# Optimization experiments

Measured on AMD Instinct MI355X. Metric: run time of the kernel, lower is better.

The kernel has to match this reference:

```python
import jax, jax.numpy as jnp
import numpy as np

DIM = 768
HEADS = 12
HEAD_DIM = DIM // HEADS
MLP_DIM = 4 * DIM
EPS = 1e-5


def setup_inputs() -> dict:
    key = jax.random.key(0)
    ks = jax.random.split(key, 8)
    s = lambda fan_in: 1.0 / np.sqrt(fan_in)
    return {
        "x": jax.random.normal(ks[0], (2, 2048, DIM), dtype=jnp.float32),
        "ln1_w": jnp.ones((DIM,), jnp.float32),
        "ln1_b": jnp.zeros((DIM,), jnp.float32),
        # weights stored [in, out]
        "qkv_w": jax.random.normal(ks[1], (DIM, 3 * DIM), jnp.float32) * s(DIM),
        "qkv_b": jnp.zeros((3 * DIM,), jnp.float32),
        "proj_w": jax.random.normal(ks[2], (DIM, DIM), jnp.float32) * s(DIM),
        "proj_b": jnp.zeros((DIM,), jnp.float32),
        "ln2_w": jnp.ones((DIM,), jnp.float32),
        "ln2_b": jnp.zeros((DIM,), jnp.float32),
        "lin1_w": jax.random.normal(ks[3], (DIM, MLP_DIM), jnp.float32) * s(DIM),
        "lin1_b": jnp.zeros((MLP_DIM,), jnp.float32),
        "lin2_w": jax.random.normal(ks[4], (MLP_DIM, DIM), jnp.float32) * s(MLP_DIM),
        "lin2_b": jnp.zeros((DIM,), jnp.float32),
    }


def _layernorm(x, w, b):
    mu = jnp.mean(x, axis=-1, keepdims=True)
    var = jnp.mean(jnp.square(x - mu), axis=-1, keepdims=True)
    return (x - mu) * jax.lax.rsqrt(var + EPS) * w + b


def _attention(x, qkv_w, qkv_b, proj_w, proj_b):
    B, N, C = x.shape
    qkv = (x @ qkv_w + qkv_b).reshape(B, N, 3, HEADS, HEAD_DIM)
    q, k, v = qkv[:, :, 0], qkv[:, :, 1], qkv[:, :, 2]  # [B, N, H, Dh]
    scale = HEAD_DIM ** -0.5
    attn = jnp.einsum("bqhd,bkhd->bhqk", q, k) * scale  # full NxN scores
    attn = jax.nn.softmax(attn, axis=-1)
    out = jnp.einsum("bhqk,bkhd->bqhd", attn, v).reshape(B, N, C)
    return out @ proj_w + proj_b


def reference(x, ln1_w, ln1_b, qkv_w, qkv_b, proj_w, proj_b,
              ln2_w, ln2_b, lin1_w, lin1_b, lin2_w, lin2_b):
    x = x + _attention(_layernorm(x, ln1_w, ln1_b), qkv_w, qkv_b, proj_w, proj_b)
    h = _layernorm(x, ln2_w, ln2_b)
    h = jax.nn.gelu(h @ lin1_w + lin1_b, approximate=False) @ lin2_w + lin2_b
    return x + h
```

## Files before the change

### kernel.cpp

```cpp
#include <hip/hip_runtime.h>
#include <hip/hip_bf16.h>
#include <math.h>

#define DIM 768
#define NTOK 4096
#define SEQ 2048
#define HEADS 12
#define HD 64

using bf16x8 = __attribute__((ext_vector_type(8))) __bf16;
using f32x4  = __attribute__((ext_vector_type(4))) float;
typedef unsigned short u16;

__device__ inline u16 f2bf(float f) {
  union { float f; unsigned u; } v; v.f = f;
  unsigned r = v.u + 0x7fffu + ((v.u >> 16) & 1u);
  return (u16)(r >> 16);
}

__device__ inline void pk2bf(float a, float b, u16* o0, u16* o1) {
  union { __hip_bfloat162 h; u16 u[2]; } cv;
  cv.h = __float22bfloat162_rn(make_float2(a, b));
  *o0 = cv.u[0];
  *o1 = cv.u[1];
}

__device__ inline float gelu_t(float x) {
  float z = x * (1.5957691216f + 0.0713548162f * x * x);
  return x / (1.0f + __expf(-z));
}

__device__ inline void gl_lds16(const u16* g, u16* l) {
  __builtin_amdgcn_global_load_lds(
      (const __attribute__((address_space(1))) unsigned int*)g,
      (__attribute__((address_space(3))) unsigned int*)l, 16, 0, 0);
}

__global__ __launch_bounds__(256) void ln_kernel(const float* __restrict__ x,
                                                 const float* __restrict__ w,
                                                 const float* __restrict__ b,
                                                 u16* __restrict__ y) {
  int row = blockIdx.x;
  int t = threadIdx.x;
  const float* xr = x + (size_t)row * DIM;
  float v0 = xr[t], v1 = xr[t + 256], v2 = xr[t + 512];
  float s = v0 + v1 + v2;
  float q = v0 * v0 + v1 * v1 + v2 * v2;
  for (int o = 32; o > 0; o >>= 1) {
    s += __shfl_down(s, o, 64);
    q += __shfl_down(q, o, 64);
  }
  __shared__ float ws_[4], wq_[4], mb[2];
  int wid = t >> 6;
  if ((t & 63) == 0) { ws_[wid] = s; wq_[wid] = q; }
  __syncthreads();
  if (t == 0) {
    float S = ws_[0] + ws_[1] + ws_[2] + ws_[3];
    float Q = wq_[0] + wq_[1] + wq_[2] + wq_[3];
    float mean = S * (1.0f / DIM);
    float var = Q * (1.0f / DIM) - mean * mean;
    mb[0] = mean;
    mb[1] = rsqrtf(var + 1e-5f);
  }
  __syncthreads();
  float mean = mb[0], rstd = mb[1];
  u16* yr = y + (size_t)row * DIM;
  yr[t]       = f2bf((v0 - mean) * rstd * w[t]       + b[t]);
  yr[t + 256] = f2bf((v1 - mean) * rstd * w[t + 256] + b[t + 256]);
  yr[t + 512] = f2bf((v2 - mean) * rstd * w[t + 512] + b[t + 512]);
}

__global__ __launch_bounds__(256) void redln_kernel(
    const float* __restrict__ P0, const float* __restrict__ P1,
    const float* __restrict__ bias, const float* __restrict__ res,
    float* __restrict__ x2, const float* __restrict__ lnw,
    const float* __restrict__ lnb, u16* __restrict__ y) {
  int row = blockIdx.x;
  int t = threadIdx.x;
  size_t off = (size_t)row * DIM;
  float v[3];
#pragma unroll
  for (int k = 0; k < 3; ++k) {
    int c = t + k * 256;
    v[k] = P0[off + c] + P1[off + c] + bias[c] + res[off + c];
    x2[off + c] = v[k];
  }
  float s = v[0] + v[1] + v[2];
  float q = v[0] * v[0] + v[1] * v[1] + v[2] * v[2];
  for (int o = 32; o > 0; o >>= 1) {
    s += __shfl_down(s, o, 64);
    q += __shfl_down(q, o, 64);
  }
  __shared__ float ws_[4], wq_[4], mb[2];
  int wid = t >> 6;
  if ((t & 63) == 0) { ws_[wid] = s; wq_[wid] = q; }
  __syncthreads();
  if (t == 0) {
    float S = ws_[0] + ws_[1] + ws_[2] + ws_[3];
    float Q = wq_[0] + wq_[1] + wq_[2] + wq_[3];
    float mean = S * (1.0f / DIM);
    float var = Q * (1.0f / DIM) - mean * mean;
    mb[0] = mean;
    mb[1] = rsqrtf(var + 1e-5f);
  }
  __syncthreads();
  float mean = mb[0], rstd = mb[1];
#pragma unroll
  for (int k = 0; k < 3; ++k) {
    int c = t + k * 256;
    y[off + c] = f2bf((v[k] - mean) * rstd * lnw[c] + lnb[c]);
  }
}

__global__ __launch_bounds__(256) void wcvt_all(
    const float* __restrict__ W0, const float* __restrict__ W1,
    const float* __restrict__ W2, const float* __restrict__ W3,
    u16* __restrict__ T0, u16* __restrict__ T1,
    u16* __restrict__ T2, u16* __restrict__ T3) {
  int id = blockIdx.x;
  const float* W; u16* Wt; int K, N, local;
  if (id < 1728)      { W = W0; Wt = T0; K = 768;  N = 2304; local = id; }
  else if (id < 2304) { W = W1; Wt = T1; K = 768;  N = 768;  local = id - 1728; }
  else if (id < 4608) { W = W2; Wt = T2; K = 768;  N = 3072; local = id - 2304; }
  else                { W = W3; Wt = T3; K = 3072; N = 768;  local = id - 4608; }
  int ntiles = N / 32;
  int n0 = (local % ntiles) * 32, k0 = (local / ntiles) * 32;
  __shared__ float tile[32][33];
  int tid = threadIdx.x;
  int c = tid & 31, r8 = tid >> 5;
#pragma unroll
  for (int p = 0; p < 4; ++p) {
    int k = r8 + p * 8;
    tile[k][c] = W[(size_t)(k0 + k) * N + n0 + c];
  }
  __syncthreads();
#pragma unroll
  for (int p = 0; p < 4; ++p) {
    int n = r8 + p * 8;
    Wt[(size_t)(n0 + n) * K + k0 + c] = f2bf(tile[c][n]);
  }
}

__global__ __launch_bounds__(256) void vtr_kernel(const u16* __restrict__ qkvB,
                                                  u16* __restrict__ vT) {
  __shared__ u16 tile[32][33];
  int v0 = blockIdx.x * 32, j0 = blockIdx.y * 32, b = blockIdx.z;
  int tid = threadIdx.x;
  int c = tid & 31, r8 = tid >> 5;
#pragma unroll
  for (int p = 0; p < 4; ++p) {
    int r = r8 + p * 8;
    tile[r][c] = qkvB[((size_t)(b * SEQ + j0 + r)) * 2304 + 1536 + v0 + c];
  }
  __syncthreads();
#pragma unroll
  for (int p = 0; p < 4; ++p) {
    int r = r8 + p * 8;
    vT[((size_t)(b * 768 + v0 + r)) * SEQ + j0 + c] = tile[c][r];
  }
}

__global__ __launch_bounds__(256) void bgemm_kernel(
    const u16* __restrict__ A, const u16* __restrict__ Bt,
    const float* __restrict__ bias, u16* __restrict__ Cb,
    int M, int N, int K, int act) {
  __shared__ __align__(16) u16 Asl[128 * 64];
  __shared__ __align__(16) u16 Bsl[128 * 64];
  int tid = threadIdx.x;
  int lane = tid & 63, wave = tid >> 6;
  int wm = wave >> 1, wn = wave & 1;
  int bm = blockIdx.y * 128, bn = blockIdx.x * 128;
  int l15 = lane & 15, quad = lane >> 4;
  int sm8 = tid >> 3;
  int kgx = (tid & 7) ^ (sm8 & 7);

  f32x4 acc[4][4] = {};
  const u16* Ap = A + (size_t)(bm + sm8) * K + kgx * 8;
  const u16* Bp = Bt + (size_t)(bn + sm8) * K + kgx * 8;
  u16* Al = &Asl[(wave * 8) * 64];
  u16* Bl = &Bsl[(wave * 8) * 64];
  int xr = l15 & 7;

  for (int k0 = 0; k0 < K; k0 += 64) {
#pragma unroll
    for (int p = 0; p < 4; ++p)
      gl_lds16(Ap + (size_t)(p * 32) * K + k0, Al + p * 32 * 64);
#pragma unroll
    for (int p = 0; p < 4; ++p)
      gl_lds16(Bp + (size_t)(p * 32) * K + k0, Bl + p * 32 * 64);
    __syncthreads();
#pragma unroll
    for (int ks = 0; ks < 2; ++ks) {
      int pu = ((ks << 2) + quad) ^ xr;
      bf16x8 af[4], bfr[4];
#pragma unroll
      for (int i = 0; i < 4; ++i) {
        af[i]  = *(const bf16x8*)&Asl[(wm * 64 + i * 16 + l15) * 64 + pu * 8];
        bfr[i] = *(const bf16x8*)&Bsl[(wn * 64 + i * 16 + l15) * 64 + pu * 8];
      }
#pragma unroll
      for (int i = 0; i < 4; ++i)
#pragma unroll
        for (int j = 0; j < 4; ++j)
          acc[i][j] = __builtin_amdgcn_mfma_f32_16x16x32_bf16(af[i], bfr[j], acc[i][j], 0, 0, 0);
    }
    __syncthreads();
  }

#pragma unroll
  for (int i = 0; i < 4; ++i) {
#pragma unroll
    for (int j = 0; j < 4; ++j) {
      int n = bn + wn * 64 + j * 16 + l15;
      float bv = bias[n];
      float val[4];
#pragma unroll
      for (int r = 0; r < 4; ++r) {
        float v = acc[i][j][r] + bv;
        val[r] = act ? gelu_t(v) : v;
      }
      u16 c0, c1, c2, c3;
      pk2bf(val[0], val[1], &c0, &c1);
      pk2bf(val[2], val[3], &c2, &c3);
      size_t mbase = (size_t)(bm + wm * 64 + i * 16 + quad * 4) * N + n;
      Cb[mbase]         = c0;
      Cb[mbase + N]     = c1;
      Cb[mbase + 2 * N] = c2;
      Cb[mbase + 3 * N] = c3;
    }
  }
}

__global__ __launch_bounds__(256) void bgemm_splitk(
    const u16* __restrict__ A, const u16* __restrict__ Bt,
    float* __restrict__ P0, float* __restrict__ P1,
    int M, int N, int K) {
  __shared__ __align__(16) u16 Asl[128 * 64];
  __shared__ __align__(16) u16 Bsl[64 * 64];
  int tid = threadIdx.x;
  int lane = tid & 63, wave = tid >> 6;
  int wm = wave >> 1, wn = wave & 1;
  int bm = blockIdx.y * 128, bn = blockIdx.x * 64;
  int l15 = lane & 15, quad = lane >> 4;
  int sm8 = tid >> 3;
  int kgx = (tid & 7) ^ (sm8 & 7);
  int half = K >> 1;
  int kbeg = blockIdx.z * half;

  f32x4 acc[4][2] = {};
  const u16* Ap = A + (size_t)(bm + sm8) * K + kbeg + kgx * 8;
  const u16* Bp = Bt + (size_t)(bn + sm8) * K + kbeg + kgx * 8;
  u16* Al = &Asl[(wave * 8) * 64];
  u16* Bl = &Bsl[(wave * 8) * 64];
  int xr = l15 & 7;

  for (int k0 = 0; k0 < half; k0 += 64) {
#pragma unroll
    for (int p = 0; p < 4; ++p)
      gl_lds16(Ap + (size_t)(p * 32) * K + k0, Al + p * 32 * 64);
#pragma unroll
    for (int p = 0; p < 2; ++p)
      gl_lds16(Bp + (size_t)(p * 32) * K + k0, Bl + p * 32 * 64);
    __syncthreads();
#pragma unroll
    for (int ks = 0; ks < 2; ++ks) {
      int pu = ((ks << 2) + quad) ^ xr;
      bf16x8 af[4], bfr[2];
#pragma unroll
      for (int i = 0; i < 4; ++i)
        af[i] = *(const bf16x8*)&Asl[(wm * 64 + i * 16 + l15) * 64 + pu * 8];
#pragma unroll
      for (int j = 0; j < 2; ++j)
        bfr[j] = *(const bf16x8*)&Bsl[(wn * 32 + j * 16 + l15) * 64 + pu * 8];
#pragma unroll
      for (int i = 0; i < 4; ++i)
#pragma unroll
        for (int j = 0; j < 2; ++j)
          acc[i][j] = __builtin_amdgcn_mfma_f32_16x16x32_bf16(af[i], bfr[j], acc[i][j], 0, 0, 0);
    }
    __syncthreads();
  }

  float* P = blockIdx.z ? P1 : P0;
#pragma unroll
  for (int i = 0; i < 4; ++i) {
#pragma unroll
    for (int j = 0; j < 2; ++j) {
      int n = bn + wn * 32 + j * 16 + l15;
#pragma unroll
      for (int r = 0; r < 4; ++r) {
        int m = bm + wm * 64 + i * 16 + quad * 4 + r;
        P[(size_t)m * N + n] = acc[i][j][r];
      }
    }
  }
}

__global__ __launch_bounds__(256) void red_kernel(
    const float* P0, const float* __restrict__ P1,
    const float* __restrict__ bias, const float* __restrict__ res,
    float* O, int Ncols) {
  int i = blockIdx.x * 256 + threadIdx.x;
  float4 a = ((const float4*)P0)[i];
  float4 b = ((const float4*)P1)[i];
  float4 r = ((const float4*)res)[i];
  int col = (i * 4) % Ncols;
  float4 bi = *(const float4*)&bias[col];
  float4 o;
  o.x = a.x + b.x + r.x + bi.x;
  o.y = a.y + b.y + r.y + bi.y;
  o.z = a.z + b.z + r.z + bi.z;
  o.w = a.w + b.w + r.w + bi.w;
  ((float4*)O)[i] = o;
}

#define AST 72
__global__ __launch_bounds__(256) void attn_kernel(const u16* __restrict__ qkv,
                                                   const u16* __restrict__ vT,
                                                   u16* __restrict__ out) {
  __shared__ __align__(16) u16 Qs[64 * 64];
  __shared__ __align__(16) u16 Ks[2][64 * 64];
  __shared__ __align__(16) u16 Vs[2][64 * 64];
  __shared__ u16 Ps[64 * AST];

  int tid = threadIdx.x;
  int lane = tid & 63, wave = tid >> 6;
  int l15 = lane & 15, quad = lane >> 4;
  int qt = blockIdx.x * 64;
  int h = blockIdx.y, b = blockIdx.z;
  size_t base = (size_t)b * SEQ;
  int srow = lane >> 3;
  int sux = (lane & 7) ^ (srow & 7);
  int r0 = wave * 16;
  const u16* qbase = qkv + (base + qt) * 2304 + h * HD;
  const u16* kbase = qkv + base * 2304 + 768 + h * HD;
  const u16* vbase = vT + ((size_t)(b * HEADS + h) * HD) * SEQ;

  gl_lds16(qbase + (size_t)(r0 + srow) * 2304 + sux * 8, Qs + r0 * 64);
  gl_lds16(qbase + (size_t)(r0 + 8 + srow) * 2304 + sux * 8, Qs + (r0 + 8) * 64);
  gl_lds16(kbase + (size_t)(r0 + srow) * 2304 + sux * 8, Ks[0] + r0 * 64);
  gl_lds16(kbase + (size_t)(r0 + 8 + srow) * 2304 + sux * 8, Ks[0] + (r0 + 8) * 64);
  gl_lds16(vbase + (size_t)(r0 + srow) * SEQ + sux * 8, Vs[0] + r0 * 64);
  gl_lds16(vbase + (size_t)(r0 + 8 + srow) * SEQ + sux * 8, Vs[0] + (r0 + 8) * 64);
  __syncthreads();

  int xr = l15 & 7;
  bf16x8 aq0 = *(const bf16x8*)&Qs[(wave * 16 + l15) * 64 + ((quad ^ xr)) * 8];
  bf16x8 aq1 = *(const bf16x8*)&Qs[(wave * 16 + l15) * 64 + (((4 + quad) ^ xr)) * 8];

  f32x4 o_acc[4] = {};
  float l_part[4] = {0.f, 0.f, 0.f, 0.f};
  int sw = l15 >> 2;

  for (int t = 0; t < 32; ++t) {
    int buf = t & 1;
    if (t < 31) {
      size_t kt1 = (size_t)(t + 1) * 64;
      gl_lds16(kbase + (kt1 + r0 + srow) * 2304 + sux * 8, Ks[buf ^ 1] + r0 * 64);
      gl_lds16(kbase + (kt1 + r0 + 8 + srow) * 2304 + sux * 8, Ks[buf ^ 1] + (r0 + 8) * 64);
      gl_lds16(vbase + (size_t)(r0 + srow) * SEQ + kt1 + sux * 8, Vs[buf ^ 1] + r0 * 64);
      gl_lds16(vbase + (size_t)(r0 + 8 + srow) * SEQ + kt1 + sux * 8, Vs[buf ^ 1] + (r0 + 8) * 64);
    }

    f32x4 s_acc[4] = {};
    __builtin_amdgcn_s_setprio(1);
#pragma unroll
    for (int jt = 0; jt < 4; ++jt) {
      bf16x8 bk0 = *(const bf16x8*)&Ks[buf][(jt * 16 + l15) * 64 + ((quad ^ xr)) * 8];
      s_acc[jt] = __builtin_amdgcn_mfma_f32_16x16x32_bf16(aq0, bk0, s_acc[jt], 0, 0, 0);
      bf16x8 bk1 = *(const bf16x8*)&Ks[buf][(jt * 16 + l15) * 64 + (((4 + quad) ^ xr)) * 8];
      s_acc[jt] = __builtin_amdgcn_mfma_f32_16x16x32_bf16(aq1, bk1, s_acc[jt], 0, 0, 0);
    }
    __builtin_amdgcn_s_setprio(0);

#pragma unroll
    for (int r = 0; r < 4; ++r) {
      float p0 = __expf(s_acc[0][r] * 0.125f);
      float p1 = __expf(s_acc[1][r] * 0.125f);
      float p2 = __expf(s_acc[2][r] * 0.125f);
      float p3 = __expf(s_acc[3][r] * 0.125f);
      l_part[r] += p0 + p1 + p2 + p3;
      u16 b0, b1, b2, b3;
      pk2bf(p0, p1, &b0, &b1);
      pk2bf(p2, p3, &b2, &b3);
      int prow = (wave * 16 + quad * 4 + r) * AST;
      Ps[prow + ((0 ^ quad) * 16) + l15] = b0;
      Ps[prow + ((1 ^ quad) * 16) + l15] = b1;
      Ps[prow + ((2 ^ quad) * 16) + l15] = b2;
      Ps[prow + ((3 ^ quad) * 16) + l15] = b3;
    }

    __builtin_amdgcn_s_setprio(1);
#pragma unroll
    for (int ks = 0; ks < 2; ++ks) {
      int blk = ks * 2 + (quad >> 1);
      bf16x8 ap = *(const bf16x8*)&Ps[(wave * 16 + l15) * AST + ((blk ^ sw) * 16) + (quad & 1) * 8];
#pragma unroll
      for (int dt = 0; dt < 4; ++dt) {
        bf16x8 bv = *(const bf16x8*)&Vs[buf][(dt * 16 + l15) * 64 + (((ks << 2) + quad) ^ xr) * 8];
        o_acc[dt] = __builtin_amdgcn_mfma_f32_16x16x32_bf16(ap, bv, o_acc[dt], 0, 0, 0);
      }
    }
    __builtin_amdgcn_s_setprio(0);
    __syncthreads();
  }

#pragma unroll
  for (int r = 0; r < 4; ++r) {
    float l = l_part[r];
    for (int msk = 1; msk < 16; msk <<= 1) l += __shfl_xor(l, msk, 64);
    l_part[r] = 1.0f / l;
  }

#pragma unroll
  for (int r = 0; r < 4; ++r) {
    size_t trow = (base + qt + wave * 16 + quad * 4 + r) * DIM + h * HD;
    u16 c0, c1, c2, c3;
    pk2bf(o_acc[0][r] * l_part[r], o_acc[1][r] * l_part[r], &c0, &c1);
    pk2bf(o_acc[2][r] * l_part[r], o_acc[3][r] * l_part[r], &c2, &c3);
    out[trow + 0 * 16 + l15] = c0;
    out[trow + 1 * 16 + l15] = c1;
    out[trow + 2 * 16 + l15] = c2;
    out[trow + 3 * 16 + l15] = c3;
  }
}

extern "C" void kernel_launch(void* const* d_in, const int* in_sizes, int n_in,
                              void* d_out, int out_size, void* d_ws, size_t ws_size,
                              hipStream_t stream) {
  const float* x     = (const float*)d_in[0];
  const float* ln1w  = (const float*)d_in[1];
  const float* ln1b  = (const float*)d_in[2];
  const float* qkvw  = (const float*)d_in[3];
  const float* qkvbi = (const float*)d_in[4];
  const float* projw = (const float*)d_in[5];
  const float* projb = (const float*)d_in[6];
  const float* ln2w  = (const float*)d_in[7];
  const float* ln2b  = (const float*)d_in[8];
  const float* l1w   = (const float*)d_in[9];
  const float* l1b   = (const float*)d_in[10];
  const float* l2w   = (const float*)d_in[11];
  const float* l2b   = (const float*)d_in[12];
  float* out = (float*)d_out;

  char* w = (char*)d_ws;
  u16*   h     = (u16*)w;   w += (size_t)NTOK * DIM * 2;
  u16*   qkvB  = (u16*)w;
  u16*   mid   = (u16*)w;   w += (size_t)NTOK * 3072 * 2;
  u16*   attnb = (u16*)w;   w += (size_t)NTOK * DIM * 2;
  float* x2    = (float*)w; w += (size_t)NTOK * DIM * 4;
  u16*   vTb   = (u16*)w;   w += (size_t)NTOK * DIM * 2;
  u16*   qkvwt = (u16*)w;   w += (size_t)DIM * 2304 * 2;
  u16*   projwt= (u16*)w;   w += (size_t)DIM * DIM * 2;
  u16*   l1wt  = (u16*)w;   w += (size_t)DIM * 3072 * 2;
  u16*   l2wt  = (u16*)w;   w += (size_t)3072 * DIM * 2;
  float* Pbuf  = (float*)w; w += (size_t)NTOK * DIM * 4;

  wcvt_all<<<6912, 256, 0, stream>>>(qkvw, projw, l1w, l2w,
                                     qkvwt, projwt, l1wt, l2wt);

  ln_kernel<<<NTOK, 256, 0, stream>>>(x, ln1w, ln1b, h);
  bgemm_kernel<<<dim3(2304 / 128, NTOK / 128), 256, 0, stream>>>(
      h, qkvwt, qkvbi, qkvB, NTOK, 2304, DIM, 0);
  vtr_kernel<<<dim3(768 / 32, SEQ / 32, 2), 256, 0, stream>>>(qkvB, vTb);
  attn_kernel<<<dim3(SEQ / 64, HEADS, 2), 256, 0, stream>>>(qkvB, vTb, attnb);

  bgemm_splitk<<<dim3(DIM / 64, NTOK / 128, 2), 256, 0, stream>>>(
      attnb, projwt, x2, Pbuf, NTOK, DIM, DIM);
  redln_kernel<<<NTOK, 256, 0, stream>>>(x2, Pbuf, projb, x, x2, ln2w, ln2b, h);

  bgemm_kernel<<<dim3(3072 / 128, NTOK / 128), 256, 0, stream>>>(
      h, l1wt, l1b, mid, NTOK, 3072, DIM, 1);

  bgemm_splitk<<<dim3(DIM / 64, NTOK / 128, 2), 256, 0, stream>>>(
      mid, l2wt, out, Pbuf, NTOK, DIM, 3072);
  red_kernel<<<NTOK * DIM / 1024, 256, 0, stream>>>(out, Pbuf, l2b, x2, out, DIM);
}
```

Baseline: 289.8 us.

## Keep attention probabilities in registers via transposed QK MFMA and permlane swaps

The QK^T MFMA now computes the transposed score tile (K as A operand), so each lane holds probabilities along the key dimension. v_permlane32/16_swap then rearranges the packed bf16 pairs straight into the PV MFMA A-operand layout. This removes the LDS round trip through the Ps buffer and reduces the row-sum reduction to two shuffles. It also switches to exp2 with a folded scale constant. The register shuffling relies on gfx950-specific permlane instructions, and the lane mapping must be exactly right for correctness.

After: 279.0 us. -3.7%, faster.

```diff
diff --git a/kernel.cpp b/kernel.cpp
--- a/kernel.cpp
+++ b/kernel.cpp
@@ -23,6 +23,19 @@
   cv.h = __float22bfloat162_rn(make_float2(a, b));
   *o0 = cv.u[0];
   *o1 = cv.u[1];
+}
+
+__device__ inline unsigned pku32(float a, float b) {
+  union { __hip_bfloat162 h; unsigned u; } cv;
+  cv.h = __float22bfloat162_rn(make_float2(a, b));
+  return cv.u;
+}
+
+__device__ inline void plane32_swap(unsigned &a, unsigned &b) {
+  asm("v_permlane32_swap_b32 %0, %1" : "+v"(a), "+v"(b));
+}
+__device__ inline void plane16_swap(unsigned &a, unsigned &b) {
+  asm("v_permlane16_swap_b32 %0, %1" : "+v"(a), "+v"(b));
 }
 
 __device__ inline float gelu_t(float x) {
@@ -314,14 +327,12 @@
   ((float4*)O)[i] = o;
 }
 
-#define AST 72
 __global__ __launch_bounds__(256) void attn_kernel(const u16* __restrict__ qkv,
                                                    const u16* __restrict__ vT,
                                                    u16* __restrict__ out) {
   __shared__ __align__(16) u16 Qs[64 * 64];
   __shared__ __align__(16) u16 Ks[2][64 * 64];
   __shared__ __align__(16) u16 Vs[2][64 * 64];
-  __shared__ u16 Ps[64 * AST];
 
   int tid = threadIdx.x;
   int lane = tid & 63, wave = tid >> 6;
@@ -349,8 +360,8 @@
   bf16x8 aq1 = *(const bf16x8*)&Qs[(wave * 16 + l15) * 64 + (((4 + quad) ^ xr)) * 8];
 
   f32x4 o_acc[4] = {};
-  float l_part[4] = {0.f, 0.f, 0.f, 0.f};
-  int sw = l15 >> 2;
+  float lsum = 0.f;
+  const float KEXP = 0.18033688011112042f;
 
   for (int t = 0; t < 32; ++t) {
     int buf = t & 1;
@@ -362,62 +373,63 @@
       gl_lds16(vbase + (size_t)(r0 + 8 + srow) * SEQ + kt1 + sux * 8, Vs[buf ^ 1] + (r0 + 8) * 64);
     }
 
-    f32x4 s_acc[4] = {};
+    f32x4 sT[4] = {};
     __builtin_amdgcn_s_setprio(1);
 #pragma unroll
     for (int jt = 0; jt < 4; ++jt) {
       bf16x8 bk0 = *(const bf16x8*)&Ks[buf][(jt * 16 + l15) * 64 + ((quad ^ xr)) * 8];
-      s_acc[jt] = __builtin_amdgcn_mfma_f32_16x16x32_bf16(aq0, bk0, s_acc[jt], 0, 0, 0);
+      sT[jt] = __builtin_amdgcn_mfma_f32_16x16x32_bf16(bk0, aq0, sT[jt], 0, 0, 0);
       bf16x8 bk1 = *(const bf16x8*)&Ks[buf][(jt * 16 + l15) * 64 + (((4 + quad) ^ xr)) * 8];
-      s_acc[jt] = __builtin_amdgcn_mfma_f32_16x16x32_bf16(aq1, bk1, s_acc[jt], 0, 0, 0);
+      sT[jt] = __builtin_amdgcn_mfma_f32_16x16x32_bf16(bk1, aq1, sT[jt], 0, 0, 0);
     }
     __builtin_amdgcn_s_setprio(0);
 
-#pragma unroll
-    for (int r = 0; r < 4; ++r) {
-      float p0 = __expf(s_acc[0][r] * 0.125f);
-      float p1 = __expf(s_acc[1][r] * 0.125f);
-      float p2 = __expf(s_acc[2][r] * 0.125f);
-      float p3 = __expf(s_acc[3][r] * 0.125f);
-      l_part[r] += p0 + p1 + p2 + p3;
-      u16 b0, b1, b2, b3;
-      pk2bf(p0, p1, &b0, &b1);
-      pk2bf(p2, p3, &b2, &b3);
-      int prow = (wave * 16 + quad * 4 + r) * AST;
-      Ps[prow + ((0 ^ quad) * 16) + l15] = b0;
-      Ps[prow + ((1 ^ quad) * 16) + l15] = b1;
-      Ps[prow + ((2 ^ quad) * 16) + l15] = b2;
-      Ps[prow + ((3 ^ quad) * 16) + l15] = b3;
+    unsigned w01[4][2];
+#pragma unroll
+    for (int jt = 0; jt < 4; ++jt) {
+      float p0 = __builtin_amdgcn_exp2f(sT[jt][0] * KEXP);
+      float p1 = __builtin_amdgcn_exp2f(sT[jt][1] * KEXP);
+      float p2 = __builtin_amdgcn_exp2f(sT[jt][2] * KEXP);
+      float p3 = __builtin_amdgcn_exp2f(sT[jt][3] * KEXP);
+      lsum += (p0 + p1) + (p2 + p3);
+      w01[jt][0] = pku32(p0, p1);
+      w01[jt][1] = pku32(p2, p3);
     }
 
     __builtin_amdgcn_s_setprio(1);
 #pragma unroll
     for (int ks = 0; ks < 2; ++ks) {
-      int blk = ks * 2 + (quad >> 1);
-      bf16x8 ap = *(const bf16x8*)&Ps[(wave * 16 + l15) * AST + ((blk ^ sw) * 16) + (quad & 1) * 8];
+      unsigned a0 = w01[2 * ks][0], b0 = w01[2 * ks + 1][0];
+      plane32_swap(a0, b0);
+      plane16_swap(a0, b0);
+      unsigned a1 = w01[2 * ks][1], b1 = w01[2 * ks + 1][1];
+      plane32_swap(a1, b1);
+      plane16_swap(a1, b1);
+      union { bf16x8 v; unsigned u[4]; } AP;
+      AP.u[0] = a0; AP.u[1] = a1; AP.u[2] = b0; AP.u[3] = b1;
 #pragma unroll
       for (int dt = 0; dt < 4; ++dt) {
         bf16x8 bv = *(const bf16x8*)&Vs[buf][(dt * 16 + l15) * 64 + (((ks << 2) + quad) ^ xr) * 8];
-        o_acc[dt] = __builtin_amdgcn_mfma_f32_16x16x32_bf16(ap, bv, o_acc[dt], 0, 0, 0);
+        o_acc[dt] = __builtin_amdgcn_mfma_f32_16x16x32_bf16(AP.v, bv, o_acc[dt], 0, 0, 0);
       }
     }
     __builtin_amdgcn_s_setprio(0);
     __syncthreads();
   }
 
-#pragma unroll
-  for (int r = 0; r < 4; ++r) {
-    float l = l_part[r];
-    for (int msk = 1; msk < 16; msk <<= 1) l += __shfl_xor(l, msk, 64);
-    l_part[r] = 1.0f / l;
-  }
+  lsum += __shfl_xor(lsum, 16, 64);
+  lsum += __shfl_xor(lsum, 32, 64);
+  float linv = 1.0f / lsum;
+  float lr[4];
+#pragma unroll
+  for (int r = 0; r < 4; ++r) lr[r] = __shfl(linv, quad * 4 + r, 64);
 
 #pragma unroll
   for (int r = 0; r < 4; ++r) {
     size_t trow = (base + qt + wave * 16 + quad * 4 + r) * DIM + h * HD;
     u16 c0, c1, c2, c3;
-    pk2bf(o_acc[0][r] * l_part[r], o_acc[1][r] * l_part[r], &c0, &c1);
-    pk2bf(o_acc[2][r] * l_part[r], o_acc[3][r] * l_part[r], &c2, &c3);
+    pk2bf(o_acc[0][r] * lr[r], o_acc[1][r] * lr[r], &c0, &c1);
+    pk2bf(o_acc[2][r] * lr[r], o_acc[3][r] * lr[r], &c2, &c3);
     out[trow + 0 * 16 + l15] = c0;
     out[trow + 1 * 16 + l15] = c1;
     out[trow + 2 * 16 + l15] = c2;
```
